# Optimization experiments

Hardware: AMD Instinct MI355X
Metric: run time of the kernel (lower is better)

Reference implementation:

```python
import jax, jax.numpy as jnp
import numpy as np

B, N, K = 8, 4096, 64
D = 256   # d_model
G = 512   # g: number of query points


def _gather(points, idx):
    # points: [B, N, C], idx: [B, G, K] -> [B, G, K, C]
    return jax.vmap(lambda p, i: p[i])(points, idx)


def _mlp(h, W1, b1, W2, b2):
    # torch Linear: y = x @ W.T + b
    return jax.nn.relu(h @ W1.T + b1) @ W2.T + b2


def setup_inputs() -> dict:
    key = jax.random.key(0)
    ks = jax.random.split(key, 12)
    s = 1.0 / np.sqrt(D)
    return {
        "xyz": jax.random.normal(ks[0], (B, N, 3), jnp.float32),
        "x": jax.random.normal(ks[1], (B, N, D), jnp.float32),
        "dist_arg_sort": jax.random.randint(ks[2], (B, N, K), 0, N),
        "Wq": jax.random.normal(ks[3], (D, D), jnp.float32) * s,
        "Wk": jax.random.normal(ks[4], (D, D), jnp.float32) * s,
        "Wv": jax.random.normal(ks[5], (D, D), jnp.float32) * s,
        "Wd1": jax.random.normal(ks[6], (D, 3), jnp.float32) * 0.5,
        "bd1": jnp.zeros((D,), jnp.float32),
        "Wd2": jax.random.normal(ks[7], (D, D), jnp.float32) * s,
        "bd2": jnp.zeros((D,), jnp.float32),
        "Wg1": jax.random.normal(ks[8], (D, D), jnp.float32) * s,
        "bg1": jnp.zeros((D,), jnp.float32),
        "Wg2": jax.random.normal(ks[9], (D, D), jnp.float32) * s,
        "bg2": jnp.zeros((D,), jnp.float32),
    }


def reference(xyz, x, dist_arg_sort, Wq, Wk, Wv, Wd1, bd1, Wd2, bd2, Wg1, bg1, Wg2, bg2):
    g_idx = jnp.sort(dist_arg_sort[:, :G], axis=-1)          # [B,G,K]
    g_xyz = _gather(xyz, g_idx)                               # [B,G,K,3]
    gq = x[:, :G] @ Wq.T                                      # [B,G,D]
    gk = _gather(x @ Wk.T, g_idx)                             # [B,G,K,D]
    gv = _gather(x @ Wv.T, g_idx)                             # [B,G,K,D]
    # positional encoding MLP on coordinate deltas
    g_pos_enc = _mlp(xyz[:, :G, None] - g_xyz, Wd1, bd1, Wd2, bd2)  # [B,G,K,D]
    # vector attention MLP
    g_attn = _mlp(gq[:, :, None] - gk + g_pos_enc, Wg1, bg1, Wg2, bg2)
    g_attn = jax.nn.softmax(g_attn / np.sqrt(D).astype(np.float32), axis=-2)
    # weighted sum over neighbor dim
    return jnp.einsum("bmnf,bmnf->bmf", g_attn, gv + g_pos_enc)  # [B,G,D]
```

## Files before the change

kernel.cpp:

```cpp
#include <hip/hip_runtime.h>

#define DEV static __device__ __forceinline__

typedef __attribute__((ext_vector_type(8))) short bf16x8;
typedef __attribute__((ext_vector_type(4))) float f32x4;
typedef __attribute__((ext_vector_type(4))) unsigned u32x4;

constexpr int BB = 8, NN = 4096, KK = 64, DD = 256, GG = 512;
constexpr int PITCH = 560;

DEV unsigned short f2b(float f){
  unsigned u = __builtin_bit_cast(unsigned, f);
  unsigned r = (u + 0x7FFFu + ((u >> 16) & 1u)) >> 16;
  return (unsigned short)r;
}
DEV float b2f(unsigned short h){
  unsigned u = ((unsigned)h) << 16;
  return __builtin_bit_cast(float, u);
}
DEV unsigned f2b2(float lo, float hi){
  unsigned r;
  asm("v_cvt_pk_bf16_f32 %0, %1, %2" : "=v"(r) : "v"(lo), "v"(hi));
  return r;
}
DEV int rof(int row, int byteoff){ return row*PITCH + byteoff; }

DEV f32x4 zero4(){ f32x4 z = {0.f, 0.f, 0.f, 0.f}; return z; }

__global__ void k_detect(const unsigned short* __restrict__ x_raw, int* __restrict__ flag){
  int lane = threadIdx.x;
  float mx = 0.f;
#pragma unroll
  for (int i = 0; i < 16; ++i) mx = fmaxf(mx, fabsf(b2f(x_raw[lane*16 + i])));
  unsigned long long big = __ballot(mx > 1e4f);
  if (lane == 0) *flag = (big == 0ull) ? 1 : 0;
}

struct PrepArgs {
  const void* src[12];
  void*       dst[12];
  int         n[12];
  int         bf16out[12];
};

__global__ void k_prep(PrepArgs P, const int* __restrict__ flagp){
  int flag = *flagp;
  long stride = (long)gridDim.x * blockDim.x;
  long gid = (long)blockIdx.x * blockDim.x + threadIdx.x;
  for (int s = 0; s < 12; ++s){
    int ns = P.n[s];
    const void* sp = P.src[s];
    if (P.bf16out[s]){
      unsigned short* dp = (unsigned short*)P.dst[s];
      for (long i = gid; i < ns; i += stride)
        dp[i] = flag ? ((const unsigned short*)sp)[i] : f2b(((const float*)sp)[i]);
    } else {
      float* dp = (float*)P.dst[s];
      for (long i = gid; i < ns; i += stride)
        dp[i] = flag ? b2f(((const unsigned short*)sp)[i]) : ((const float*)sp)[i];
    }
  }
}

DEV void preB(const unsigned short* __restrict__ Wt, int lane, int c0, bf16x8 b0[2]){
  const unsigned short* wbase = Wt + (c0 + (lane & 15))*DD + (lane >> 4)*8;
  b0[0] = *(const bf16x8*)(wbase);
  b0[1] = *(const bf16x8*)(wbase + 16*DD);
}

DEV void gemm64(const char* sbuf, const unsigned short* __restrict__ Wt,
                int lane, int c0, f32x4 acc[4][4]){
  const int lrow = lane & 15, lk = lane >> 4;
  const unsigned short* wbase = Wt + (c0 + lrow)*DD + lk*8;
  bf16x8 B[3][4];
#pragma unroll
  for (int nf = 0; nf < 4; ++nf) B[0][nf] = *(const bf16x8*)(wbase + nf*16*DD);
#pragma unroll
  for (int nf = 0; nf < 4; ++nf) B[1][nf] = *(const bf16x8*)(wbase + nf*16*DD + 32);
#pragma unroll
  for (int ks = 0; ks < 8; ++ks){
    bf16x8 a[4];
#pragma unroll
    for (int mf = 0; mf < 4; ++mf)
      a[mf] = *(const bf16x8*)(sbuf + rof(mf*16 + lrow, ks*64 + lk*16));
    if (ks < 6){
#pragma unroll
      for (int nf = 0; nf < 4; ++nf)
        B[(ks + 2) % 3][nf] = *(const bf16x8*)(wbase + nf*16*DD + (ks + 2)*32);
    }
    __builtin_amdgcn_s_setprio(1);
#pragma unroll
    for (int mf = 0; mf < 4; ++mf)
#pragma unroll
      for (int nf = 0; nf < 4; ++nf)
        acc[mf][nf] = __builtin_amdgcn_mfma_f32_16x16x32_bf16(a[mf], B[ks % 3][nf], acc[mf][nf], 0, 0, 0);
    __builtin_amdgcn_s_setprio(0);
  }
}

DEV void gemm32(const char* sbuf, const unsigned short* __restrict__ Wt,
                int lane, int c0, f32x4 acc[4][2], const bf16x8 b0[2]){
  const int lrow = lane & 15, lk = lane >> 4;
  const unsigned short* wbase = Wt + (c0 + lrow)*DD + lk*8;
  bf16x8 B[3][2];
  B[0][0] = b0[0]; B[0][1] = b0[1];
#pragma unroll
  for (int nf = 0; nf < 2; ++nf)
    B[1][nf] = *(const bf16x8*)(wbase + nf*16*DD + 32);
#pragma unroll
  for (int ks = 0; ks < 8; ++ks){
    bf16x8 a[4];
#pragma unroll
    for (int mf = 0; mf < 4; ++mf)
      a[mf] = *(const bf16x8*)(sbuf + rof(mf*16 + lrow, ks*64 + lk*16));
    if (ks < 6){
#pragma unroll
      for (int nf = 0; nf < 2; ++nf)
        B[(ks + 2) % 3][nf] = *(const bf16x8*)(wbase + nf*16*DD + (ks + 2)*32);
    }
    __builtin_amdgcn_s_setprio(1);
#pragma unroll
    for (int mf = 0; mf < 4; ++mf)
#pragma unroll
      for (int nf = 0; nf < 2; ++nf)
        acc[mf][nf] = __builtin_amdgcn_mfma_f32_16x16x32_bf16(a[mf], B[ks % 3][nf], acc[mf][nf], 0, 0, 0);
    __builtin_amdgcn_s_setprio(0);
  }
}

__global__ __launch_bounds__(256, 2) void k_gemmA(
    const void* __restrict__ x_in,
    const unsigned short* __restrict__ Wq_b, const unsigned short* __restrict__ Wk_b,
    const unsigned short* __restrict__ Wv_b,
    unsigned short* __restrict__ ktab, unsigned short* __restrict__ vtab,
    float* __restrict__ gq, const int* __restrict__ flagp){
  __shared__ __align__(16) char sA[64*PITCH];
  const int tid = threadIdx.x, lane = tid & 63, wv = tid >> 6;
  const int flag = *flagp;
  const long row0 = (long)blockIdx.x * 64;
  const int b = (int)(row0 >> 12), n0 = (int)(row0 & 4095);

#pragma unroll
  for (int it = 0; it < 8; ++it){
    int r = (tid >> 5) + it*8;
    int f0 = (tid & 31)*8;
    bf16x8 v;
    if (flag){
      v = *(const bf16x8*)((const unsigned short*)x_in + (row0 + r)*DD + f0);
    } else {
      const float* xp = (const float*)x_in + (row0 + r)*DD + f0;
      f32x4 lo = *(const f32x4*)xp;
      f32x4 hi = *(const f32x4*)(xp + 4);
      u32x4 t;
#pragma unroll
      for (int e = 0; e < 2; ++e){ t[e] = f2b2(lo[2*e], lo[2*e+1]); t[e+2] = f2b2(hi[2*e], hi[2*e+1]); }
      v = __builtin_bit_cast(bf16x8, t);
    }
    *(bf16x8*)(sA + rof(r, f0*2)) = v;
  }
  __syncthreads();

  const int c0 = wv*64;
  const int nout = (n0 < GG) ? 3 : 2;
  for (int o = 0; o < nout; ++o){
    const unsigned short* Wt = (o == 0) ? Wk_b : (o == 1) ? Wv_b : Wq_b;
    f32x4 acc[4][4];
#pragma unroll
    for (int mf = 0; mf < 4; ++mf)
#pragma unroll
      for (int nf = 0; nf < 4; ++nf) acc[mf][nf] = zero4();
    gemm64(sA, Wt, lane, c0, acc);
#pragma unroll
    for (int mf = 0; mf < 4; ++mf)
#pragma unroll
      for (int nf = 0; nf < 4; ++nf)
#pragma unroll
        for (int r = 0; r < 4; ++r){
          int grow = mf*16 + (lane >> 4)*4 + r;
          int col = c0 + nf*16 + (lane & 15);
          float v = acc[mf][nf][r];
          if (o == 0)      ktab[(row0 + grow)*DD + col] = f2b(v);
          else if (o == 1) vtab[(row0 + grow)*DD + col] = f2b(v);
          else             gq[((long)b*GG + n0 + grow)*DD + col] = v;
        }
  }
}

__global__ __launch_bounds__(512, 4) void k_attn(
    const unsigned short* __restrict__ ktab, const unsigned short* __restrict__ vtab,
    const float* __restrict__ gq, const float* __restrict__ xyzf, const int* __restrict__ didx,
    const unsigned short* __restrict__ Wd2_b, const unsigned short* __restrict__ Wg1_b,
    const unsigned short* __restrict__ Wg2_b,
    const float* __restrict__ Wd1f, const float* __restrict__ bd1f, const float* __restrict__ bd2f,
    const float* __restrict__ bg1f, const float* __restrict__ bg2f,
    void* __restrict__ out, const int* __restrict__ flagp){
  __shared__ __align__(16) char S[64*PITCH];
  __shared__ __align__(16) char U[64*PITCH];
  __shared__ float s_gq[256];
  __shared__ float s_delta[64*3];

  const int tid = threadIdx.x, lane = tid & 63, wv = tid >> 6;
  const int gang = tid >> 5;
  const int f0 = (tid & 31)*8;
  const int flag = *flagp;
  int wg = blockIdx.x;
  wg = (wg & 7)*512 + (wg >> 3);
  const int b = wg >> 9, g = wg & 511;
  const long bN = (long)b * NN;

  int jrow[4];
  {
    const int* dptr = didx + (bN + g)*KK + gang*4;
#pragma unroll
    for (int it = 0; it < 4; ++it) jrow[it] = dptr[it];
  }
  if (tid < 256) s_gq[tid] = gq[((long)b*GG + g)*DD + tid];
  if (tid < 64){
    int j = didx[(bN + g)*KK + tid];
    long qb = (bN + g)*3, jb = (bN + j)*3;
#pragma unroll
    for (int c = 0; c < 3; ++c) s_delta[tid*3 + c] = xyzf[qb + c] - xyzf[jb + c];
  }
  f32x4 w1v[6];
  {
    const f32x4* wp = (const f32x4*)(Wd1f + f0*3);
#pragma unroll
    for (int q = 0; q < 6; ++q) w1v[q] = wp[q];
  }
  f32x4 b1lo = *(const f32x4*)(bd1f + f0), b1hi = *(const f32x4*)(bd1f + f0 + 4);
  const int c0 = wv*32;
  float bg2lo = bg2f[c0 + (lane & 15)];
  float bg2hi = bg2f[c0 + 16 + (lane & 15)];
  __syncthreads();

  bf16x8 b0d2[2];
  preB(Wd2_b, lane, c0, b0d2);
#pragma unroll
  for (int it = 0; it < 4; ++it){
    int r = gang*4 + it;
    float d0 = s_delta[r*3], d1 = s_delta[r*3+1], d2 = s_delta[r*3+2];
    float h[8];
#pragma unroll
    for (int e = 0; e < 8; ++e){
      float bias = (e < 4) ? b1lo[e] : b1hi[e-4];
      float w0 = w1v[(e*3+0) >> 2][(e*3+0) & 3];
      float w1 = w1v[(e*3+1) >> 2][(e*3+1) & 3];
      float w2 = w1v[(e*3+2) >> 2][(e*3+2) & 3];
      h[e] = fmaxf(fmaf(d0, w0, fmaf(d1, w1, fmaf(d2, w2, bias))), 0.f);
    }
    u32x4 t;
#pragma unroll
    for (int q = 0; q < 4; ++q) t[q] = f2b2(h[2*q], h[2*q+1]);
    *(bf16x8*)(S + rof(r, f0*2)) = __builtin_bit_cast(bf16x8, t);
  }

  bf16x8 kreg[4];
#pragma unroll
  for (int it = 0; it < 4; ++it)
    kreg[it] = *(const bf16x8*)(ktab + (bN + jrow[it])*DD + f0);
  __syncthreads();

  {
    f32x4 acc[4][2];
#pragma unroll
    for (int mf = 0; mf < 4; ++mf)
#pragma unroll
      for (int nf = 0; nf < 2; ++nf) acc[mf][nf] = zero4();
    gemm32(S, Wd2_b, lane, c0, acc, b0d2);
#pragma unroll
    for (int nf = 0; nf < 2; ++nf){
      float bias = bd2f[c0 + nf*16 + (lane & 15)];
#pragma unroll
      for (int mf = 0; mf < 4; ++mf){
        int row = mf*16 + (lane >> 4)*4;
        int col = c0 + nf*16 + (lane & 15);
#pragma unroll
        for (int h = 0; h < 2; ++h){
          unsigned pk = f2b2(acc[mf][nf][2*h] + bias, acc[mf][nf][2*h+1] + bias);
          *(unsigned short*)(U + rof(row + 2*h,     col*2)) = (unsigned short)(pk & 0xffff);
          *(unsigned short*)(U + rof(row + 2*h + 1, col*2)) = (unsigned short)(pk >> 16);
        }
      }
    }
  }
  __syncthreads();

  bf16x8 b0g1[2];
  preB(Wg1_b, lane, c0, b0g1);
#pragma unroll
  for (int it = 0; it < 4; ++it){
    int r = gang*4 + it;
    bf16x8 p8 = *(const bf16x8*)(U + rof(r, f0*2));
    float v[8];
#pragma unroll
    for (int e = 0; e < 8; ++e)
      v[e] = s_gq[f0 + e] - b2f((unsigned short)kreg[it][e]) + b2f((unsigned short)p8[e]);
    u32x4 t;
#pragma unroll
    for (int q = 0; q < 4; ++q) t[q] = f2b2(v[2*q], v[2*q+1]);
    *(bf16x8*)(S + rof(r, f0*2)) = __builtin_bit_cast(bf16x8, t);
  }
  __syncthreads();

  bf16x8 b0g2[2];
  {
    f32x4 acc[4][2];
#pragma unroll
    for (int mf = 0; mf < 4; ++mf)
#pragma unroll
      for (int nf = 0; nf < 2; ++nf) acc[mf][nf] = zero4();
    gemm32(S, Wg1_b, lane, c0, acc, b0g1);
    preB(Wg2_b, lane, c0, b0g2);
    __syncthreads();
#pragma unroll
    for (int nf = 0; nf < 2; ++nf){
      float bias = bg1f[c0 + nf*16 + (lane & 15)];
#pragma unroll
      for (int mf = 0; mf < 4; ++mf){
        int row = mf*16 + (lane >> 4)*4;
        int col = c0 + nf*16 + (lane & 15);
#pragma unroll
        for (int h = 0; h < 2; ++h){
          unsigned pk = f2b2(fmaxf(acc[mf][nf][2*h] + bias, 0.f),
                             fmaxf(acc[mf][nf][2*h+1] + bias, 0.f));
          *(unsigned short*)(S + rof(row + 2*h,     col*2)) = (unsigned short)(pk & 0xffff);
          *(unsigned short*)(S + rof(row + 2*h + 1, col*2)) = (unsigned short)(pk >> 16);
        }
      }
    }
  }
  __syncthreads();

  f32x4 lg[4][2];
#pragma unroll
  for (int mf = 0; mf < 4; ++mf)
#pragma unroll
    for (int nf = 0; nf < 2; ++nf) lg[mf][nf] = zero4();
  gemm32(S, Wg2_b, lane, c0, lg, b0g2);
  __syncthreads();

  bf16x8 vreg[4];
#pragma unroll
  for (int it = 0; it < 4; ++it)
    vreg[it] = *(const bf16x8*)(vtab + (bN + jrow[it])*DD + f0);

#pragma unroll
  for (int nf = 0; nf < 2; ++nf){
    float bias = (nf == 0) ? bg2lo : bg2hi;
    float m = -1e30f;
#pragma unroll
    for (int mf = 0; mf < 4; ++mf)
#pragma unroll
      for (int r = 0; r < 4; ++r){ lg[mf][nf][r] += bias; m = fmaxf(m, lg[mf][nf][r]); }
    m = fmaxf(m, __shfl_xor(m, 16));
    m = fmaxf(m, __shfl_xor(m, 32));
    float s = 0.f;
#pragma unroll
    for (int mf = 0; mf < 4; ++mf)
#pragma unroll
      for (int r = 0; r < 4; ++r){
        float e = __expf((lg[mf][nf][r] - m) * 0.0625f);
        lg[mf][nf][r] = e; s += e;
      }
    s += __shfl_xor(s, 16);
    s += __shfl_xor(s, 32);
    float inv = 1.f / s;
#pragma unroll
    for (int mf = 0; mf < 4; ++mf){
      int row = mf*16 + (lane >> 4)*4;
      int col = c0 + nf*16 + (lane & 15);
#pragma unroll
      for (int h = 0; h < 2; ++h){
        unsigned pk = f2b2(lg[mf][nf][2*h] * inv, lg[mf][nf][2*h+1] * inv);
        *(unsigned short*)(S + rof(row + 2*h,     col*2)) = (unsigned short)(pk & 0xffff);
        *(unsigned short*)(S + rof(row + 2*h + 1, col*2)) = (unsigned short)(pk >> 16);
      }
    }
  }
  __syncthreads();

  {
    float accv[8];
#pragma unroll
    for (int e = 0; e < 8; ++e) accv[e] = 0.f;
#pragma unroll
    for (int kk2 = 0; kk2 < 4; ++kk2){
      int row = gang*4 + kk2;
      bf16x8 w8 = *(const bf16x8*)(S + rof(row, f0*2));
      bf16x8 p8 = *(const bf16x8*)(U + rof(row, f0*2));
#pragma unroll
      for (int e = 0; e < 8; ++e)
        accv[e] = fmaf(b2f((unsigned short)w8[e]),
                       b2f((unsigned short)vreg[kk2][e]) + b2f((unsigned short)p8[e]), accv[e]);
    }
    float* red = (float*)(S + gang*4*PITCH);
    f32x4 lo = {accv[0], accv[1], accv[2], accv[3]};
    f32x4 hi = {accv[4], accv[5], accv[6], accv[7]};
    *(f32x4*)(red + f0)     = lo;
    *(f32x4*)(red + f0 + 4) = hi;
  }
  __syncthreads();
  if (tid < 256){
    float v = 0.f;
#pragma unroll
    for (int p = 0; p < 16; ++p) v += *(const float*)(S + p*4*PITCH + tid*4);
    long oi = ((long)b*GG + g)*DD + tid;
    if (flag) ((unsigned short*)out)[oi] = f2b(v);
    else      ((float*)out)[oi] = v;
  }
}

extern "C" void kernel_launch(void* const* d_in, const int* in_sizes, int n_in,
                              void* d_out, int out_size, void* d_ws, size_t ws_size,
                              hipStream_t stream){
  char* ws = (char*)d_ws;
  int* flag = (int*)ws;
  unsigned short* ktab = (unsigned short*)(ws + 256);
  unsigned short* vtab = ktab + (size_t)BB*NN*DD;
  float* gq   = (float*)(vtab + (size_t)BB*NN*DD);
  float* xyzf = gq + (size_t)BB*GG*DD;
  unsigned short* Wq_b  = (unsigned short*)(xyzf + (size_t)BB*NN*3);
  unsigned short* Wk_b  = Wq_b  + DD*DD;
  unsigned short* Wv_b  = Wk_b  + DD*DD;
  unsigned short* Wd2_b = Wv_b  + DD*DD;
  unsigned short* Wg1_b = Wd2_b + DD*DD;
  unsigned short* Wg2_b = Wg1_b + DD*DD;
  float* Wd1f = (float*)(Wg2_b + DD*DD);
  float* bd1f = Wd1f + DD*3;
  float* bd2f = bd1f + DD;
  float* bg1f = bd2f + DD;
  float* bg2f = bg1f + DD;

  k_detect<<<1, 64, 0, stream>>>((const unsigned short*)d_in[1], flag);

  PrepArgs P;
  const int wsrc[6] = {3, 4, 5, 8, 10, 12};
  unsigned short* wdst[6] = {Wq_b, Wk_b, Wv_b, Wd2_b, Wg1_b, Wg2_b};
  for (int i = 0; i < 6; ++i){ P.src[i] = d_in[wsrc[i]]; P.dst[i] = wdst[i]; P.n[i] = DD*DD; P.bf16out[i] = 1; }
  P.src[6]  = d_in[0];  P.dst[6]  = xyzf; P.n[6]  = BB*NN*3; P.bf16out[6]  = 0;
  P.src[7]  = d_in[6];  P.dst[7]  = Wd1f; P.n[7]  = DD*3;    P.bf16out[7]  = 0;
  P.src[8]  = d_in[7];  P.dst[8]  = bd1f; P.n[8]  = DD;      P.bf16out[8]  = 0;
  P.src[9]  = d_in[9];  P.dst[9]  = bd2f; P.n[9]  = DD;      P.bf16out[9]  = 0;
  P.src[10] = d_in[11]; P.dst[10] = bg1f; P.n[10] = DD;      P.bf16out[10] = 0;
  P.src[11] = d_in[13]; P.dst[11] = bg2f; P.n[11] = DD;      P.bf16out[11] = 0;
  k_prep<<<256, 256, 0, stream>>>(P, flag);

  k_gemmA<<<512, 256, 0, stream>>>(d_in[1], Wq_b, Wk_b, Wv_b, ktab, vtab, gq, flag);

  k_attn<<<4096, 512, 0, stream>>>(ktab, vtab, gq, xyzf, (const int*)d_in[2],
      Wd2_b, Wg1_b, Wg2_b, Wd1f, bd1f, bd2f, bg1f, bg2f, d_out, flag);
}
```

Before: 272.0 us.

## Process two query points per workgroup and prefetch next point's indices

Each workgroup now handles two consecutive query points in a loop, with grid halved to 2048 blocks. During the first point's attention, it prefetches the neighbour indices, query vector and coordinate deltas for the second point into registers, then writes them to shared memory after a barrier. This amortizes per-block setup such as the Wd1 and bias loads, and hides index-load latency. In exchange each block runs longer and there are fewer blocks for load balance.

Measured after the change: 413.3 us. 1.52x slower.

```diff
diff --git a/kernel.cpp b/kernel.cpp
--- a/kernel.cpp
+++ b/kernel.cpp
@@ -204,23 +204,11 @@
   const int f0 = (tid & 31)*8;
   const int flag = *flagp;
   int wg = blockIdx.x;
-  wg = (wg & 7)*512 + (wg >> 3);
-  const int b = wg >> 9, g = wg & 511;
+  wg = (wg & 7)*256 + (wg >> 3);
+  const int b = wg >> 8;
+  const int g0 = (wg & 255)*2;
   const long bN = (long)b * NN;
 
-  int jrow[4];
-  {
-    const int* dptr = didx + (bN + g)*KK + gang*4;
-#pragma unroll
-    for (int it = 0; it < 4; ++it) jrow[it] = dptr[it];
-  }
-  if (tid < 256) s_gq[tid] = gq[((long)b*GG + g)*DD + tid];
-  if (tid < 64){
-    int j = didx[(bN + g)*KK + tid];
-    long qb = (bN + g)*3, jb = (bN + j)*3;
-#pragma unroll
-    for (int c = 0; c < 3; ++c) s_delta[tid*3 + c] = xyzf[qb + c] - xyzf[jb + c];
-  }
   f32x4 w1v[6];
   {
     const f32x4* wp = (const f32x4*)(Wd1f + f0*3);
@@ -231,182 +219,228 @@
   const int c0 = wv*32;
   float bg2lo = bg2f[c0 + (lane & 15)];
   float bg2hi = bg2f[c0 + 16 + (lane & 15)];
+
+  int jrow[4];
+  {
+    const int* dptr = didx + (bN + g0)*KK + gang*4;
+#pragma unroll
+    for (int it = 0; it < 4; ++it) jrow[it] = dptr[it];
+  }
+  if (tid < 256) s_gq[tid] = gq[((long)b*GG + g0)*DD + tid];
+  if (tid < 64){
+    int j = didx[(bN + g0)*KK + tid];
+    long qb = (bN + g0)*3, jb = (bN + j)*3;
+#pragma unroll
+    for (int c = 0; c < 3; ++c) s_delta[tid*3 + c] = xyzf[qb + c] - xyzf[jb + c];
+  }
   __syncthreads();
 
-  bf16x8 b0d2[2];
-  preB(Wd2_b, lane, c0, b0d2);
-#pragma unroll
-  for (int it = 0; it < 4; ++it){
-    int r = gang*4 + it;
-    float d0 = s_delta[r*3], d1 = s_delta[r*3+1], d2 = s_delta[r*3+2];
-    float h[8];
-#pragma unroll
-    for (int e = 0; e < 8; ++e){
-      float bias = (e < 4) ? b1lo[e] : b1hi[e-4];
-      float w0 = w1v[(e*3+0) >> 2][(e*3+0) & 3];
-      float w1 = w1v[(e*3+1) >> 2][(e*3+1) & 3];
-      float w2 = w1v[(e*3+2) >> 2][(e*3+2) & 3];
-      h[e] = fmaxf(fmaf(d0, w0, fmaf(d1, w1, fmaf(d2, w2, bias))), 0.f);
-    }
-    u32x4 t;
-#pragma unroll
-    for (int q = 0; q < 4; ++q) t[q] = f2b2(h[2*q], h[2*q+1]);
-    *(bf16x8*)(S + rof(r, f0*2)) = __builtin_bit_cast(bf16x8, t);
-  }
-
-  bf16x8 kreg[4];
-#pragma unroll
-  for (int it = 0; it < 4; ++it)
-    kreg[it] = *(const bf16x8*)(ktab + (bN + jrow[it])*DD + f0);
-  __syncthreads();
-
-  {
-    f32x4 acc[4][2];
-#pragma unroll
-    for (int mf = 0; mf < 4; ++mf)
-#pragma unroll
-      for (int nf = 0; nf < 2; ++nf) acc[mf][nf] = zero4();
-    gemm32(S, Wd2_b, lane, c0, acc, b0d2);
+  int jrow_n[4];
+  float gq_n = 0.f, d_n0 = 0.f, d_n1 = 0.f, d_n2 = 0.f;
+
+  for (int gi = 0; gi < 2; ++gi){
+    const int g = g0 + gi;
+
+    bf16x8 b0d2[2];
+    preB(Wd2_b, lane, c0, b0d2);
+#pragma unroll
+    for (int it = 0; it < 4; ++it){
+      int r = gang*4 + it;
+      float d0 = s_delta[r*3], d1 = s_delta[r*3+1], d2 = s_delta[r*3+2];
+      float h[8];
+#pragma unroll
+      for (int e = 0; e < 8; ++e){
+        float bias = (e < 4) ? b1lo[e] : b1hi[e-4];
+        float w0 = w1v[(e*3+0) >> 2][(e*3+0) & 3];
+        float w1 = w1v[(e*3+1) >> 2][(e*3+1) & 3];
+        float w2 = w1v[(e*3+2) >> 2][(e*3+2) & 3];
+        h[e] = fmaxf(fmaf(d0, w0, fmaf(d1, w1, fmaf(d2, w2, bias))), 0.f);
+      }
+      u32x4 t;
+#pragma unroll
+      for (int q = 0; q < 4; ++q) t[q] = f2b2(h[2*q], h[2*q+1]);
+      *(bf16x8*)(S + rof(r, f0*2)) = __builtin_bit_cast(bf16x8, t);
+    }
+
+    bf16x8 kreg[4];
+#pragma unroll
+    for (int it = 0; it < 4; ++it)
+      kreg[it] = *(const bf16x8*)(ktab + (bN + jrow[it])*DD + f0);
+    __syncthreads();
+
+    {
+      f32x4 acc[4][2];
+#pragma unroll
+      for (int mf = 0; mf < 4; ++mf)
+#pragma unroll
+        for (int nf = 0; nf < 2; ++nf) acc[mf][nf] = zero4();
+      gemm32(S, Wd2_b, lane, c0, acc, b0d2);
+#pragma unroll
+      for (int nf = 0; nf < 2; ++nf){
+        float bias = bd2f[c0 + nf*16 + (lane & 15)];
+#pragma unroll
+        for (int mf = 0; mf < 4; ++mf){
+          int row = mf*16 + (lane >> 4)*4;
+          int col = c0 + nf*16 + (lane & 15);
+#pragma unroll
+          for (int h = 0; h < 2; ++h){
+            unsigned pk = f2b2(acc[mf][nf][2*h] + bias, acc[mf][nf][2*h+1] + bias);
+            *(unsigned short*)(U + rof(row + 2*h,     col*2)) = (unsigned short)(pk & 0xffff);
+            *(unsigned short*)(U + rof(row + 2*h + 1, col*2)) = (unsigned short)(pk >> 16);
+          }
+        }
+      }
+    }
+    __syncthreads();
+
+    bf16x8 b0g1[2];
+    preB(Wg1_b, lane, c0, b0g1);
+#pragma unroll
+    for (int it = 0; it < 4; ++it){
+      int r = gang*4 + it;
+      bf16x8 p8 = *(const bf16x8*)(U + rof(r, f0*2));
+      float v[8];
+#pragma unroll
+      for (int e = 0; e < 8; ++e)
+        v[e] = s_gq[f0 + e] - b2f((unsigned short)kreg[it][e]) + b2f((unsigned short)p8[e]);
+      u32x4 t;
+#pragma unroll
+      for (int q = 0; q < 4; ++q) t[q] = f2b2(v[2*q], v[2*q+1]);
+      *(bf16x8*)(S + rof(r, f0*2)) = __builtin_bit_cast(bf16x8, t);
+    }
+
+    if (gi == 0){
+      const int gn = g0 + 1;
+      const int* dptr = didx + (bN + gn)*KK + gang*4;
+#pragma unroll
+      for (int it = 0; it < 4; ++it) jrow_n[it] = dptr[it];
+      if (tid < 256) gq_n = gq[((long)b*GG + gn)*DD + tid];
+      if (tid < 64){
+        int j = didx[(bN + gn)*KK + tid];
+        long qb = (bN + gn)*3, jb = (bN + j)*3;
+        d_n0 = xyzf[qb + 0] - xyzf[jb + 0];
+        d_n1 = xyzf[qb + 1] - xyzf[jb + 1];
+        d_n2 = xyzf[qb + 2] - xyzf[jb + 2];
+      }
+    }
+    __syncthreads();
+
+    if (gi == 0){
+      if (tid < 256) s_gq[tid] = gq_n;
+      if (tid < 64){ s_delta[tid*3] = d_n0; s_delta[tid*3+1] = d_n1; s_delta[tid*3+2] = d_n2; }
+    }
+
+    bf16x8 b0g2[2];
+    {
+      f32x4 acc[4][2];
+#pragma unroll
+      for (int mf = 0; mf < 4; ++mf)
+#pragma unroll
+        for (int nf = 0; nf < 2; ++nf) acc[mf][nf] = zero4();
+      gemm32(S, Wg1_b, lane, c0, acc, b0g1);
+      preB(Wg2_b, lane, c0, b0g2);
+      __syncthreads();
+#pragma unroll
+      for (int nf = 0; nf < 2; ++nf){
+        float bias = bg1f[c0 + nf*16 + (lane & 15)];
+#pragma unroll
+        for (int mf = 0; mf < 4; ++mf){
+          int row = mf*16 + (lane >> 4)*4;
+          int col = c0 + nf*16 + (lane & 15);
+#pragma unroll
+          for (int h = 0; h < 2; ++h){
+            unsigned pk = f2b2(fmaxf(acc[mf][nf][2*h] + bias, 0.f),
+                               fmaxf(acc[mf][nf][2*h+1] + bias, 0.f));
+            *(unsigned short*)(S + rof(row + 2*h,     col*2)) = (unsigned short)(pk & 0xffff);
+            *(unsigned short*)(S + rof(row + 2*h + 1, col*2)) = (unsigned short)(pk >> 16);
+          }
+        }
+      }
+    }
+    __syncthreads();
+
+    f32x4 lg[4][2];
+#pragma unroll
+    for (int mf = 0; mf < 4; ++mf)
+#pragma unroll
+      for (int nf = 0; nf < 2; ++nf) lg[mf][nf] = zero4();
+    gemm32(S, Wg2_b, lane, c0, lg, b0g2);
+    __syncthreads();
+
+    bf16x8 vreg[4];
+#pragma unroll
+    for (int it = 0; it < 4; ++it)
+      vreg[it] = *(const bf16x8*)(vtab + (bN + jrow[it])*DD + f0);
+
 #pragma unroll
     for (int nf = 0; nf < 2; ++nf){
-      float bias = bd2f[c0 + nf*16 + (lane & 15)];
+      float bias = (nf == 0) ? bg2lo : bg2hi;
+      float m = -1e30f;
+#pragma unroll
+      for (int mf = 0; mf < 4; ++mf)
+#pragma unroll
+        for (int r = 0; r < 4; ++r){ lg[mf][nf][r] += bias; m = fmaxf(m, lg[mf][nf][r]); }
+      m = fmaxf(m, __shfl_xor(m, 16));
+      m = fmaxf(m, __shfl_xor(m, 32));
+      float s = 0.f;
+#pragma unroll
+      for (int mf = 0; mf < 4; ++mf)
+#pragma unroll
+        for (int r = 0; r < 4; ++r){
+          float e = __expf((lg[mf][nf][r] - m) * 0.0625f);
+          lg[mf][nf][r] = e; s += e;
+        }
+      s += __shfl_xor(s, 16);
+      s += __shfl_xor(s, 32);
+      float inv = 1.f / s;
 #pragma unroll
       for (int mf = 0; mf < 4; ++mf){
         int row = mf*16 + (lane >> 4)*4;
         int col = c0 + nf*16 + (lane & 15);
 #pragma unroll
         for (int h = 0; h < 2; ++h){
-          unsigned pk = f2b2(acc[mf][nf][2*h] + bias, acc[mf][nf][2*h+1] + bias);
-          *(unsigned short*)(U + rof(row + 2*h,     col*2)) = (unsigned short)(pk & 0xffff);
-          *(unsigned short*)(U + rof(row + 2*h + 1, col*2)) = (unsigned short)(pk >> 16);
-        }
-      }
-    }
-  }
-  __syncthreads();
-
-  bf16x8 b0g1[2];
-  preB(Wg1_b, lane, c0, b0g1);
-#pragma unroll
-  for (int it = 0; it < 4; ++it){
-    int r = gang*4 + it;
-    bf16x8 p8 = *(const bf16x8*)(U + rof(r, f0*2));
-    float v[8];
-#pragma unroll
-    for (int e = 0; e < 8; ++e)
-      v[e] = s_gq[f0 + e] - b2f((unsigned short)kreg[it][e]) + b2f((unsigned short)p8[e]);
-    u32x4 t;
-#pragma unroll
-    for (int q = 0; q < 4; ++q) t[q] = f2b2(v[2*q], v[2*q+1]);
-    *(bf16x8*)(S + rof(r, f0*2)) = __builtin_bit_cast(bf16x8, t);
-  }
-  __syncthreads();
-
-  bf16x8 b0g2[2];
-  {
-    f32x4 acc[4][2];
-#pragma unroll
-    for (int mf = 0; mf < 4; ++mf)
-#pragma unroll
-      for (int nf = 0; nf < 2; ++nf) acc[mf][nf] = zero4();
-    gemm32(S, Wg1_b, lane, c0, acc, b0g1);
-    preB(Wg2_b, lane, c0, b0g2);
-    __syncthreads();
-#pragma unroll
-    for (int nf = 0; nf < 2; ++nf){
-      float bias = bg1f[c0 + nf*16 + (lane & 15)];
-#pragma unroll
-      for (int mf = 0; mf < 4; ++mf){
-        int row = mf*16 + (lane >> 4)*4;
-        int col = c0 + nf*16 + (lane & 15);
-#pragma unroll
-        for (int h = 0; h < 2; ++h){
-          unsigned pk = f2b2(fmaxf(acc[mf][nf][2*h] + bias, 0.f),
-                             fmaxf(acc[mf][nf][2*h+1] + bias, 0.f));
+          unsigned pk = f2b2(lg[mf][nf][2*h] * inv, lg[mf][nf][2*h+1] * inv);
           *(unsigned short*)(S + rof(row + 2*h,     col*2)) = (unsigned short)(pk & 0xffff);
           *(unsigned short*)(S + rof(row + 2*h + 1, col*2)) = (unsigned short)(pk >> 16);
         }
       }
     }
-  }
-  __syncthreads();
-
-  f32x4 lg[4][2];
-#pragma unroll
-  for (int mf = 0; mf < 4; ++mf)
-#pragma unroll
-    for (int nf = 0; nf < 2; ++nf) lg[mf][nf] = zero4();
-  gemm32(S, Wg2_b, lane, c0, lg, b0g2);
-  __syncthreads();
-
-  bf16x8 vreg[4];
-#pragma unroll
-  for (int it = 0; it < 4; ++it)
-    vreg[it] = *(const bf16x8*)(vtab + (bN + jrow[it])*DD + f0);
-
-#pragma unroll
-  for (int nf = 0; nf < 2; ++nf){
-    float bias = (nf == 0) ? bg2lo : bg2hi;
-    float m = -1e30f;
-#pragma unroll
-    for (int mf = 0; mf < 4; ++mf)
-#pragma unroll
-      for (int r = 0; r < 4; ++r){ lg[mf][nf][r] += bias; m = fmaxf(m, lg[mf][nf][r]); }
-    m = fmaxf(m, __shfl_xor(m, 16));
-    m = fmaxf(m, __shfl_xor(m, 32));
-    float s = 0.f;
-#pragma unroll
-    for (int mf = 0; mf < 4; ++mf)
-#pragma unroll
-      for (int r = 0; r < 4; ++r){
-        float e = __expf((lg[mf][nf][r] - m) * 0.0625f);
-        lg[mf][nf][r] = e; s += e;
-      }
-    s += __shfl_xor(s, 16);
-    s += __shfl_xor(s, 32);
-    float inv = 1.f / s;
-#pragma unroll
-    for (int mf = 0; mf < 4; ++mf){
-      int row = mf*16 + (lane >> 4)*4;
-      int col = c0 + nf*16 + (lane & 15);
-#pragma unroll
-      for (int h = 0; h < 2; ++h){
-        unsigned pk = f2b2(lg[mf][nf][2*h] * inv, lg[mf][nf][2*h+1] * inv);
-        *(unsigned short*)(S + rof(row + 2*h,     col*2)) = (unsigned short)(pk & 0xffff);
-        *(unsigned short*)(S + rof(row + 2*h + 1, col*2)) = (unsigned short)(pk >> 16);
-      }
-    }
-  }
-  __syncthreads();
-
-  {
-    float accv[8];
-#pragma unroll
-    for (int e = 0; e < 8; ++e) accv[e] = 0.f;
-#pragma unroll
-    for (int kk2 = 0; kk2 < 4; ++kk2){
-      int row = gang*4 + kk2;
-      bf16x8 w8 = *(const bf16x8*)(S + rof(row, f0*2));
-      bf16x8 p8 = *(const bf16x8*)(U + rof(row, f0*2));
-#pragma unroll
-      for (int e = 0; e < 8; ++e)
-        accv[e] = fmaf(b2f((unsigned short)w8[e]),
-                       b2f((unsigned short)vreg[kk2][e]) + b2f((unsigned short)p8[e]), accv[e]);
-    }
-    float* red = (float*)(S + gang*4*PITCH);
-    f32x4 lo = {accv[0], accv[1], accv[2], accv[3]};
-    f32x4 hi = {accv[4], accv[5], accv[6], accv[7]};
-    *(f32x4*)(red + f0)     = lo;
-    *(f32x4*)(red + f0 + 4) = hi;
-  }
-  __syncthreads();
-  if (tid < 256){
-    float v = 0.f;
-#pragma unroll
-    for (int p = 0; p < 16; ++p) v += *(const float*)(S + p*4*PITCH + tid*4);
-    long oi = ((long)b*GG + g)*DD + tid;
-    if (flag) ((unsigned short*)out)[oi] = f2b(v);
-    else      ((float*)out)[oi] = v;
+    __syncthreads();
+
+    {
+      float accv[8];
+#pragma unroll
+      for (int e = 0; e < 8; ++e) accv[e] = 0.f;
+#pragma unroll
+      for (int kk2 = 0; kk2 < 4; ++kk2){
+        int row = gang*4 + kk2;
+        bf16x8 w8 = *(const bf16x8*)(S + rof(row, f0*2));
+        bf16x8 p8 = *(const bf16x8*)(U + rof(row, f0*2));
+#pragma unroll
+        for (int e = 0; e < 8; ++e)
+          accv[e] = fmaf(b2f((unsigned short)w8[e]),
+                         b2f((unsigned short)vreg[kk2][e]) + b2f((unsigned short)p8[e]), accv[e]);
+      }
+      float* red = (float*)(S + gang*4*PITCH);
+      f32x4 lo = {accv[0], accv[1], accv[2], accv[3]};
+      f32x4 hi = {accv[4], accv[5], accv[6], accv[7]};
+      *(f32x4*)(red + f0)     = lo;
+      *(f32x4*)(red + f0 + 4) = hi;
+    }
+    __syncthreads();
+    if (tid < 256){
+      float v = 0.f;
+#pragma unroll
+      for (int p = 0; p < 16; ++p) v += *(const float*)(S + p*4*PITCH + tid*4);
+      long oi = ((long)b*GG + g)*DD + tid;
+      if (flag) ((unsigned short*)out)[oi] = f2b(v);
+      else      ((float*)out)[oi] = v;
+    }
+    if (gi == 0){
+      __syncthreads();
+#pragma unroll
+      for (int it = 0; it < 4; ++it) jrow[it] = jrow_n[it];
+    }
   }
 }
 
@@ -447,6 +481,6 @@
 
   k_gemmA<<<512, 256, 0, stream>>>(d_in[1], Wq_b, Wk_b, Wv_b, ktab, vtab, gq, flag);
 
-  k_attn<<<4096, 512, 0, stream>>>(ktab, vtab, gq, xyzf, (const int*)d_in[2],
+  k_attn<<<2048, 512, 0, stream>>>(ktab, vtab, gq, xyzf, (const int*)d_in[2],
       Wd2_b, Wg1_b, Wg2_b, Wd1f, bd1f, bd2f, bg1f, bg2f, d_out, flag);
 }
```
